# Optimization experiments

Hardware: AMD Instinct MI355X
Metric: run time of the kernel (lower is better)

Reference implementation:

```python
import jax, jax.numpy as jnp
import numpy as np

B = 64            # decode batch (one new token per sequence)
H = 32            # query heads
HKV = 2           # kv heads (multi_query_group_num)
D = 128           # head_size (kv_channels)
HID = 4096        # hidden size
ROT = D // 2      # ChatGLM applies rotary to first half of head dims
BLOCK = 16        # paged-cache block size
NBLK = 16384      # total blocks
MAX_S = 4096
ROPE_BASE = 10000.0


def setup_inputs() -> dict:
    key = jax.random.key(0)
    ks = jax.random.split(key, 8)
    hidden_states = jax.random.normal(ks[0], (B, HID), jnp.float32)
    wqkv = jax.random.normal(ks[1], (H * D + 2 * HKV * D, HID), jnp.float32) * 0.02
    wdense = jax.random.normal(ks[2], (HID, H * D), jnp.float32) * 0.02
    k_cache = jax.random.normal(ks[3], (NBLK, BLOCK, HKV, D), jnp.float32)
    v_cache = jax.random.normal(ks[4], (NBLK, BLOCK, HKV, D), jnp.float32)
    # disjoint block tables: sequence b owns blocks [b*256, (b+1)*256)
    block_tables = jnp.arange(B * (MAX_S // BLOCK), dtype=jnp.int32).reshape(B, MAX_S // BLOCK)
    input_lengths = jax.random.randint(ks[5], (B,), 1024, MAX_S + 1, dtype=jnp.int32)
    # slot of the current token = position input_lengths-1 within its block table
    pos = input_lengths - 1
    slots = block_tables[jnp.arange(B), pos // BLOCK] * BLOCK + pos % BLOCK
    return {"hidden_states": hidden_states, "wqkv": wqkv, "wdense": wdense,
            "k_cache": k_cache, "v_cache": v_cache, "block_tables": block_tables,
            "slots": slots, "input_lengths": input_lengths, "max_s": MAX_S}


def _apply_rope(x, positions):
    # x: [B, h, D]; GPT-J interleaved rope on first ROT dims (ChatGLM style)
    inv_freq = 1.0 / (ROPE_BASE ** (jnp.arange(0, ROT, 2, dtype=jnp.float32) / ROT))  # [ROT/2]
    ang = positions.astype(jnp.float32)[:, None] * inv_freq[None, :]                  # [B, ROT/2]
    c = jnp.cos(ang)[:, None, :]  # [B,1,ROT/2]
    s = jnp.sin(ang)[:, None, :]
    xr = x[..., :ROT].reshape(*x.shape[:-1], ROT // 2, 2)
    x0, x1 = xr[..., 0], xr[..., 1]
    rot = jnp.stack([x0 * c - x1 * s, x1 * c + x0 * s], axis=-1).reshape(*x.shape[:-1], ROT)
    return jnp.concatenate([rot, x[..., ROT:]], axis=-1)


def reference(hidden_states, wqkv, wdense, k_cache, v_cache, block_tables, slots, input_lengths, max_s):
    G = H // HKV
    scale = D ** -0.5
    positions = input_lengths - 1

    qkv = hidden_states @ wqkv.T                                   # [B, 4608]
    q, k, v = jnp.split(qkv, [H * D, H * D + HKV * D], axis=1)
    q = q.reshape(B, H, D)
    k = k.reshape(B, HKV, D)
    v = v.reshape(B, HKV, D)

    q = _apply_rope(q, positions)
    k = _apply_rope(k, positions)

    # reshape_and_cache: scatter current token's K/V into the paged cache
    kc = k_cache.reshape(NBLK * BLOCK, HKV, D).at[slots].set(k)
    vc = v_cache.reshape(NBLK * BLOCK, HKV, D).at[slots].set(v)

    # paged attention: gather per-sequence KV via block tables
    s_idx = jnp.arange(max_s)
    flat = block_tables[:, s_idx // BLOCK] * BLOCK + s_idx % BLOCK  # [B, S]
    K = kc[flat]                                                    # [B, S, HKV, D]
    V = vc[flat]

    q4 = q.reshape(B, HKV, G, D).astype(jnp.float32)
    scores = jnp.einsum('bkgd,bskd->bkgs', q4, K.astype(jnp.float32)) * scale  # [B,HKV,G,S]
    mask = s_idx[None, :] < input_lengths[:, None]                  # [B, S]
    scores = jnp.where(mask[:, None, None, :], scores, -jnp.inf)
    probs = jax.nn.softmax(scores, axis=-1)
    out = jnp.einsum('bkgs,bskd->bkgd', probs, V.astype(jnp.float32))  # [B,HKV,G,D]
    out = out.reshape(B, H * D).astype(hidden_states.dtype)
    return out @ wdense.T
```

## Files before the change

kernel.cpp:

```cpp
#include <hip/hip_runtime.h>
#include <math.h>

#define KDIM 4096
#define SPLITS 8
#define WAYS 32
#define MAXPB 256
#define NQKV 4608
#define NDENSE 4096
#define KSPLIT 8
#define KRANGE 512

typedef __attribute__((ext_vector_type(8))) short bh8;
typedef __attribute__((ext_vector_type(4))) float f32x4;

__device__ __forceinline__ short f2bf(float x) {
    union { float f; unsigned u; } v; v.f = x;
    unsigned r = v.u + 0x7FFFu + ((v.u >> 16) & 1u);
    return (short)(r >> 16);
}
__device__ __forceinline__ float bf2f(short h) {
    union { unsigned u; float f; } v;
    v.u = ((unsigned)(unsigned short)h) << 16;
    return v.f;
}

__device__ __forceinline__ void rope_rotate(float& x0, float& x1, int j, int pos) {
    double inv = pow(10000.0, -(double)j / 32.0);
    double ang = (double)pos * inv;
    float c = (float)cos(ang), s = (float)sin(ang);
    float r0 = x0 * c - x1 * s;
    float r1 = x1 * c + x0 * s;
    x0 = r0; x1 = r1;
}

__global__ __launch_bounds__(256) void prep_hilo(
    const float* __restrict__ x, unsigned short* __restrict__ hi,
    unsigned short* __restrict__ lo)
{
    const int i = (blockIdx.x * 256 + threadIdx.x) * 4;
    float4 v = *(const float4*)&x[i];
    unsigned short h4[4], l4[4];
    float vf[4] = {v.x, v.y, v.z, v.w};
    #pragma unroll
    for (int j = 0; j < 4; ++j) {
        short hh = f2bf(vf[j]);
        h4[j] = (unsigned short)hh;
        l4[j] = (unsigned short)f2bf(vf[j] - bf2f(hh));
    }
    *(ushort4*)&hi[i] = make_ushort4(h4[0], h4[1], h4[2], h4[3]);
    *(ushort4*)&lo[i] = make_ushort4(l4[0], l4[1], l4[2], l4[3]);
}

__global__ __launch_bounds__(256) void gemm_mfma(
    const unsigned short* __restrict__ A_hi, const unsigned short* __restrict__ A_lo,
    const float* __restrict__ W, float* __restrict__ part, int N)
{
    const int tid = threadIdx.x;
    const int wv = tid >> 6;
    const int l = tid & 63;
    const int lr = l & 15;
    const int h = l >> 4;
    const int n0 = blockIdx.x * 64 + wv * 16;
    const int k0 = blockIdx.y * KRANGE;

    const float* wrow = &W[(size_t)(n0 + lr) * KDIM + h * 8];
    const unsigned short* pah[4];
    const unsigned short* pal[4];
    #pragma unroll
    for (int mt = 0; mt < 4; ++mt) {
        pah[mt] = &A_hi[(mt * 16 + lr) * KDIM + h * 8];
        pal[mt] = &A_lo[(mt * 16 + lr) * KDIM + h * 8];
    }

    f32x4 acc[4];
    #pragma unroll
    for (int mt = 0; mt < 4; ++mt) acc[mt] = (f32x4){0.f, 0.f, 0.f, 0.f};

    float4 wc0, wc1, wn0, wn1;
    bh8 ahc[4], alc[4], ahn[4], aln[4];

    wc0 = *(const float4*)&wrow[k0];
    wc1 = *(const float4*)&wrow[k0 + 4];
    #pragma unroll
    for (int mt = 0; mt < 4; ++mt) {
        ahc[mt] = *(const bh8*)&pah[mt][k0];
        alc[mt] = *(const bh8*)&pal[mt][k0];
    }

    for (int kt = 0; kt < KRANGE / 32; ++kt) {
        if (kt + 1 < KRANGE / 32) {
            const int kn = k0 + (kt + 1) * 32;
            wn0 = *(const float4*)&wrow[kn];
            wn1 = *(const float4*)&wrow[kn + 4];
            #pragma unroll
            for (int mt = 0; mt < 4; ++mt) {
                ahn[mt] = *(const bh8*)&pah[mt][kn];
                aln[mt] = *(const bh8*)&pal[mt][kn];
            }
        }
        bh8 whi, wlo;
        float wf[8] = {wc0.x, wc0.y, wc0.z, wc0.w, wc1.x, wc1.y, wc1.z, wc1.w};
        #pragma unroll
        for (int e = 0; e < 8; ++e) {
            short hh = f2bf(wf[e]);
            whi[e] = hh;
            wlo[e] = f2bf(wf[e] - bf2f(hh));
        }
        #pragma unroll
        for (int mt = 0; mt < 4; ++mt) {
            acc[mt] = __builtin_amdgcn_mfma_f32_16x16x32_bf16(ahc[mt], whi, acc[mt], 0, 0, 0);
            acc[mt] = __builtin_amdgcn_mfma_f32_16x16x32_bf16(alc[mt], whi, acc[mt], 0, 0, 0);
            acc[mt] = __builtin_amdgcn_mfma_f32_16x16x32_bf16(ahc[mt], wlo, acc[mt], 0, 0, 0);
        }
        wc0 = wn0; wc1 = wn1;
        #pragma unroll
        for (int mt = 0; mt < 4; ++mt) { ahc[mt] = ahn[mt]; alc[mt] = aln[mt]; }
    }

    const int ks = blockIdx.y;
    #pragma unroll
    for (int mt = 0; mt < 4; ++mt) {
        const int m = mt * 16 + h * 4;
        #pragma unroll
        for (int j = 0; j < 4; ++j)
            part[((size_t)ks * 64 + m + j) * N + n0 + lr] = acc[mt][j];
    }
}

__global__ __launch_bounds__(256) void reduce_qkv(
    const float* __restrict__ part, const int* __restrict__ lens,
    float* __restrict__ q_rope, float* __restrict__ knew, float* __restrict__ vnew)
{
    const int b = blockIdx.y;
    const int c0 = (blockIdx.x * 256 + threadIdx.x) * 2;
    float x0 = 0.f, x1 = 0.f;
    #pragma unroll
    for (int ks = 0; ks < KSPLIT; ++ks) {
        float2 v = *(const float2*)&part[((size_t)ks * 64 + b) * NQKV + c0];
        x0 += v.x; x1 += v.y;
    }
    const int pos = lens[b] - 1;
    if (c0 < 4096) {
        const int d = c0 & 127;
        if (d < 64) rope_rotate(x0, x1, d >> 1, pos);
        q_rope[(size_t)b * 4096 + c0] = x0;
        q_rope[(size_t)b * 4096 + c0 + 1] = x1;
    } else if (c0 < 4352) {
        const int kidx = c0 - 4096, kh = kidx >> 7, d = kidx & 127;
        if (d < 64) rope_rotate(x0, x1, d >> 1, pos);
        knew[(b * 2 + kh) * 128 + d] = x0;
        knew[(b * 2 + kh) * 128 + d + 1] = x1;
    } else {
        const int vidx = c0 - 4352, kh = vidx >> 7, d = vidx & 127;
        vnew[(b * 2 + kh) * 128 + d] = x0;
        vnew[(b * 2 + kh) * 128 + d + 1] = x1;
    }
}

__global__ __launch_bounds__(256) void attn_mfma(
    const float* __restrict__ qr, const float* __restrict__ knew,
    const float* __restrict__ vnew, const float* __restrict__ kcache,
    const float* __restrict__ vcache, const int* __restrict__ bt,
    const int* __restrict__ lens, float* __restrict__ pO, float* __restrict__ pML)
{
    const int split = blockIdx.x;
    const int kh = blockIdx.y;
    const int b = blockIdx.z;
    const int tid = threadIdx.x;
    const int wv = tid >> 6;
    const int l = tid & 63;
    const int g = l & 15;
    const int h = l >> 4;
    const int way = split * 4 + wv;

    __shared__ unsigned int sP[4][256];
    __shared__ float sO[3][16][132];
    __shared__ float sML[3][2][16];

    const int len = lens[b];
    const int nchunks = (len + 31) >> 5;
    const size_t nbase = ((size_t)(b * 2 + kh)) * 128;

    const float scale = 0.08838834764831845f;
    bh8 qf[4];
    {
        const float* qrow = &qr[((size_t)(b * 32 + kh * 16 + g)) * 128 + h * 8];
        #pragma unroll
        for (int dc = 0; dc < 4; ++dc) {
            float4 a = *(const float4*)&qrow[dc * 32];
            float4 c = *(const float4*)&qrow[dc * 32 + 4];
            qf[dc][0] = f2bf(a.x * scale); qf[dc][1] = f2bf(a.y * scale);
            qf[dc][2] = f2bf(a.z * scale); qf[dc][3] = f2bf(a.w * scale);
            qf[dc][4] = f2bf(c.x * scale); qf[dc][5] = f2bf(c.y * scale);
            qf[dc][6] = f2bf(c.z * scale); qf[dc][7] = f2bf(c.w * scale);
        }
    }

    float m = -INFINITY, lacc = 0.f;
    f32x4 oacc[8];
    #pragma unroll
    for (int dt = 0; dt < 8; ++dt) oacc[dt] = (f32x4){0.f, 0.f, 0.f, 0.f};

    for (int c = way; c < nchunks; c += WAYS) {
        const int s0 = c * 32;
        const int blk0 = bt[b * MAXPB + 2 * c];
        const int blk1 = bt[b * MAXPB + 2 * c + 1];

        const float* rowK0 = (s0 + g == len - 1) ? &knew[nbase]
            : &kcache[(((size_t)blk0 * 16 + g) * 2 + kh) * 128];
        const float* rowK1 = (s0 + 16 + g == len - 1) ? &knew[nbase]
            : &kcache[(((size_t)blk1 * 16 + g) * 2 + kh) * 128];
        float4 k0[8], k1[8];
        #pragma unroll
        for (int dc = 0; dc < 4; ++dc) {
            k0[2*dc]   = *(const float4*)&rowK0[dc * 32 + h * 8];
            k0[2*dc+1] = *(const float4*)&rowK0[dc * 32 + h * 8 + 4];
            k1[2*dc]   = *(const float4*)&rowK1[dc * 32 + h * 8];
            k1[2*dc+1] = *(const float4*)&rowK1[dc * 32 + h * 8 + 4];
        }

        float vv[8][8];
        #pragma unroll
        for (int e = 0; e < 8; ++e) {
            const int p = h * 8 + e;
            const int s = s0 + p;
            const float* rowV = (s == len - 1) ? &vnew[nbase]
                : &vcache[(((size_t)(p < 16 ? blk0 : blk1) * 16 + (p & 15)) * 2 + kh) * 128];
            #pragma unroll
            for (int dt = 0; dt < 8; ++dt)
                vv[e][dt] = rowV[dt * 16 + g];
        }

        f32x4 sa0 = (f32x4){0.f,0.f,0.f,0.f};
        f32x4 sa1 = (f32x4){0.f,0.f,0.f,0.f};
        #pragma unroll
        for (int dc = 0; dc < 4; ++dc) {
            bh8 a0, a1;
            a0[0]=f2bf(k0[2*dc].x);   a0[1]=f2bf(k0[2*dc].y);
            a0[2]=f2bf(k0[2*dc].z);   a0[3]=f2bf(k0[2*dc].w);
            a0[4]=f2bf(k0[2*dc+1].x); a0[5]=f2bf(k0[2*dc+1].y);
            a0[6]=f2bf(k0[2*dc+1].z); a0[7]=f2bf(k0[2*dc+1].w);
            a1[0]=f2bf(k1[2*dc].x);   a1[1]=f2bf(k1[2*dc].y);
            a1[2]=f2bf(k1[2*dc].z);   a1[3]=f2bf(k1[2*dc].w);
            a1[4]=f2bf(k1[2*dc+1].x); a1[5]=f2bf(k1[2*dc+1].y);
            a1[6]=f2bf(k1[2*dc+1].z); a1[7]=f2bf(k1[2*dc+1].w);
            sa0 = __builtin_amdgcn_mfma_f32_16x16x32_bf16(a0, qf[dc], sa0, 0, 0, 0);
            sa1 = __builtin_amdgcn_mfma_f32_16x16x32_bf16(a1, qf[dc], sa1, 0, 0, 0);
        }

        float sc[8];
        #pragma unroll
        for (int j = 0; j < 4; ++j) {
            sc[j]     = (s0 + 4*h + j      < len) ? sa0[j] : -INFINITY;
            sc[4 + j] = (s0 + 16 + 4*h + j < len) ? sa1[j] : -INFINITY;
        }
        float tmax = sc[0];
        #pragma unroll
        for (int j = 1; j < 8; ++j) tmax = fmaxf(tmax, sc[j]);
        tmax = fmaxf(tmax, __shfl_xor(tmax, 16));
        tmax = fmaxf(tmax, __shfl_xor(tmax, 32));
        const float m_new = fmaxf(m, tmax);
        const float corr = expf(m - m_new);
        float pe[8], ls = 0.f;
        #pragma unroll
        for (int j = 0; j < 8; ++j) { pe[j] = expf(sc[j] - m_new); ls += pe[j]; }
        ls += __shfl_xor(ls, 16);
        ls += __shfl_xor(ls, 32);
        lacc = lacc * corr + ls;
        m = m_new;
        #pragma unroll
        for (int dt = 0; dt < 8; ++dt) {
            oacc[dt][0] *= corr; oacc[dt][1] *= corr;
            oacc[dt][2] *= corr; oacc[dt][3] *= corr;
        }

        unsigned int* myP = sP[wv];
        #pragma unroll
        for (int ph = 0; ph < 2; ++ph)
            #pragma unroll
            for (int t2 = 0; t2 < 2; ++t2) {
                unsigned lo = (unsigned short)f2bf(pe[ph*4 + 2*t2]);
                unsigned hi = (unsigned short)f2bf(pe[ph*4 + 2*t2 + 1]);
                myP[g * 16 + ph * 8 + 2 * h + t2] = lo | (hi << 16);
            }
        asm volatile("s_waitcnt lgkmcnt(0)" ::: "memory");
        bh8 pf = *(const bh8*)&myP[g * 16 + 4 * h];

        #pragma unroll
        for (int dt = 0; dt < 8; ++dt) {
            bh8 av;
            #pragma unroll
            for (int e = 0; e < 8; ++e) av[e] = f2bf(vv[e][dt]);
            oacc[dt] = __builtin_amdgcn_mfma_f32_16x16x32_bf16(av, pf, oacc[dt], 0, 0, 0);
        }
    }

    if (wv > 0) {
        #pragma unroll
        for (int dt = 0; dt < 8; ++dt)
            #pragma unroll
            for (int j = 0; j < 4; ++j)
                sO[wv-1][g][dt*16 + 4*h + j] = oacc[dt][j];
        if (l < 16) {
            sML[wv-1][0][g] = m;
            sML[wv-1][1][g] = lacc;
        }
    }
    __syncthreads();
    if (wv == 0) {
        float M = m;
        #pragma unroll
        for (int i = 0; i < 3; ++i) M = fmaxf(M, sML[i][0][g]);
        const float w0 = expf(m - M);
        float L = lacc * w0;
        float wi[3];
        #pragma unroll
        for (int i = 0; i < 3; ++i) {
            wi[i] = expf(sML[i][0][g] - M);
            L += sML[i][1][g] * wi[i];
        }
        size_t base = ((((size_t)(b * 2 + kh)) * SPLITS + split) * 16 + g) * 128;
        #pragma unroll
        for (int dt = 0; dt < 8; ++dt)
            #pragma unroll
            for (int j = 0; j < 4; ++j) {
                float o = oacc[dt][j] * w0;
                #pragma unroll
                for (int i = 0; i < 3; ++i)
                    o += sO[i][g][dt*16 + 4*h + j] * wi[i];
                pO[base + dt*16 + 4*h + j] = o;
            }
        if (l < 16) {
            size_t mb = ((((size_t)(b * 2 + kh)) * SPLITS + split) * 16 + g) * 2;
            pML[mb] = M;
            pML[mb + 1] = L;
        }
    }
}

__global__ __launch_bounds__(256) void attn_combine(
    const float* __restrict__ pO, const float* __restrict__ pML,
    unsigned short* __restrict__ a_hi, unsigned short* __restrict__ a_lo)
{
    const int bk = blockIdx.x;
    const int tid = threadIdx.x;
    const int g = tid >> 4;
    const int dh = tid & 15;

    float ms[SPLITS], ls[SPLITS];
    float M = -INFINITY;
    #pragma unroll
    for (int s = 0; s < SPLITS; ++s) {
        size_t mb = (((size_t)bk * SPLITS + s) * 16 + g) * 2;
        ms[s] = pML[mb]; ls[s] = pML[mb + 1];
        M = fmaxf(M, ms[s]);
    }
    float L = 0.f;
    #pragma unroll
    for (int s = 0; s < SPLITS; ++s) L += ls[s] * expf(ms[s] - M);

    float acc[8] = {0, 0, 0, 0, 0, 0, 0, 0};
    #pragma unroll
    for (int s = 0; s < SPLITS; ++s) {
        float wgt = expf(ms[s] - M);
        const float* src = &pO[(((size_t)bk * SPLITS + s) * 16 + g) * 128 + dh * 8];
        #pragma unroll
        for (int r = 0; r < 8; ++r) acc[r] += wgt * src[r];
    }
    const float invL = 1.f / L;
    const int b = bk >> 1, kh = bk & 1;
    const size_t idx = (size_t)b * 4096 + (kh * 16 + g) * 128 + dh * 8;
    unsigned short hbuf[8], lbuf[8];
    #pragma unroll
    for (int r = 0; r < 8; ++r) {
        float o = acc[r] * invL;
        short hh = f2bf(o);
        hbuf[r] = (unsigned short)hh;
        lbuf[r] = (unsigned short)f2bf(o - bf2f(hh));
    }
    *(int4*)&a_hi[idx] = *(int4*)hbuf;
    *(int4*)&a_lo[idx] = *(int4*)lbuf;
}

__global__ __launch_bounds__(256) void reduce_dense(
    const float* __restrict__ part, float* __restrict__ out)
{
    const int b = blockIdx.y;
    const int col = (blockIdx.x * 256 + threadIdx.x) * 4;
    float4 s = make_float4(0.f, 0.f, 0.f, 0.f);
    #pragma unroll
    for (int ks = 0; ks < KSPLIT; ++ks) {
        float4 v = *(const float4*)&part[((size_t)ks * 64 + b) * NDENSE + col];
        s.x += v.x; s.y += v.y; s.z += v.z; s.w += v.w;
    }
    *(float4*)&out[(size_t)b * 4096 + col] = s;
}

extern "C" void kernel_launch(void* const* d_in, const int* in_sizes, int n_in,
                              void* d_out, int out_size, void* d_ws, size_t ws_size,
                              hipStream_t stream) {
    const float* hidden = (const float*)d_in[0];
    const float* wqkv   = (const float*)d_in[1];
    const float* wdense = (const float*)d_in[2];
    const float* kcache = (const float*)d_in[3];
    const float* vcache = (const float*)d_in[4];
    const int*   bt     = (const int*)d_in[5];
    const int*   lens   = (const int*)d_in[7];
    float* out = (float*)d_out;

    float* ws     = (float*)d_ws;
    float* q_rope = ws;
    float* k_new  = ws + 262144;
    float* v_new  = ws + 278528;
    unsigned short* hiloA = (unsigned short*)(ws + 294912);
    unsigned short* A_hi = hiloA;
    unsigned short* A_lo = hiloA + 262144;
    float* regX   = ws + 557056;
    float* pO     = regX;
    float* pML    = ws + 2916352;

    prep_hilo<<<dim3(256), dim3(256), 0, stream>>>(hidden, A_hi, A_lo);
    gemm_mfma<<<dim3(NQKV / 64, KSPLIT), dim3(256), 0, stream>>>(
        A_hi, A_lo, wqkv, regX, NQKV);
    reduce_qkv<<<dim3(9, 64), dim3(256), 0, stream>>>(
        regX, lens, q_rope, k_new, v_new);
    attn_mfma<<<dim3(SPLITS, 2, 64), dim3(256), 0, stream>>>(
        q_rope, k_new, v_new, kcache, vcache, bt, lens, pO, pML);
    attn_combine<<<dim3(128), dim3(256), 0, stream>>>(pO, pML, A_hi, A_lo);
    gemm_mfma<<<dim3(NDENSE / 64, KSPLIT), dim3(256), 0, stream>>>(
        A_hi, A_lo, wdense, regX, NDENSE);
    reduce_dense<<<dim3(4, 64), dim3(256), 0, stream>>>(regX, out);
}
```

Measured before the change: 211.5 us.

## Pre-pack activations in MFMA fragment order and double split-K for GEMMs

After: 169.7 us (median of 2 runs). -19.7%, faster.

```diff
diff --git a/kernel.cpp b/kernel.cpp
--- a/kernel.cpp
+++ b/kernel.cpp
@@ -7,8 +7,8 @@
 #define MAXPB 256
 #define NQKV 4608
 #define NDENSE 4096
-#define KSPLIT 8
-#define KRANGE 512
+#define KSPLIT 16
+#define KRANGE 256
 
 typedef __attribute__((ext_vector_type(8))) short bh8;
 typedef __attribute__((ext_vector_type(4))) float f32x4;
@@ -33,22 +33,30 @@
     x0 = r0; x1 = r1;
 }
 
-__global__ __launch_bounds__(256) void prep_hilo(
+__global__ __launch_bounds__(256) void prep_hilo_pk(
     const float* __restrict__ x, unsigned short* __restrict__ hi,
     unsigned short* __restrict__ lo)
 {
-    const int i = (blockIdx.x * 256 + threadIdx.x) * 4;
-    float4 v = *(const float4*)&x[i];
-    unsigned short h4[4], l4[4];
-    float vf[4] = {v.x, v.y, v.z, v.w};
-    #pragma unroll
-    for (int j = 0; j < 4; ++j) {
-        short hh = f2bf(vf[j]);
-        h4[j] = (unsigned short)hh;
-        l4[j] = (unsigned short)f2bf(vf[j] - bf2f(hh));
-    }
-    *(ushort4*)&hi[i] = make_ushort4(h4[0], h4[1], h4[2], h4[3]);
-    *(ushort4*)&lo[i] = make_ushort4(l4[0], l4[1], l4[2], l4[3]);
+    const int id = blockIdx.x * 256 + threadIdx.x;
+    const int lane = id & 63;
+    const int mtkt = id >> 6;
+    const int mt = mtkt & 3;
+    const int kt = mtkt >> 2;
+    const int m = mt * 16 + (lane & 15);
+    const int kk = kt * 32 + (lane >> 4) * 8;
+    const float* src = &x[(size_t)m * KDIM + kk];
+    float4 a = *(const float4*)src;
+    float4 b = *(const float4*)(src + 4);
+    float vf[8] = {a.x, a.y, a.z, a.w, b.x, b.y, b.z, b.w};
+    unsigned short hbuf[8], lbuf[8];
+    #pragma unroll
+    for (int e = 0; e < 8; ++e) {
+        short hh = f2bf(vf[e]);
+        hbuf[e] = (unsigned short)hh;
+        lbuf[e] = (unsigned short)f2bf(vf[e] - bf2f(hh));
+    }
+    *(int4*)&hi[(size_t)id * 8] = *(int4*)hbuf;
+    *(int4*)&lo[(size_t)id * 8] = *(int4*)lbuf;
 }
 
 __global__ __launch_bounds__(256) void gemm_mfma(
@@ -61,45 +69,45 @@
     const int lr = l & 15;
     const int h = l >> 4;
     const int n0 = blockIdx.x * 64 + wv * 16;
-    const int k0 = blockIdx.y * KRANGE;
+    const int ks = blockIdx.y;
+    const int k0 = ks * KRANGE;
 
     const float* wrow = &W[(size_t)(n0 + lr) * KDIM + h * 8];
-    const unsigned short* pah[4];
-    const unsigned short* pal[4];
+    const size_t abase = (size_t)ks * 8 * 4 * 512 + (size_t)l * 8;
+
+    f32x4 acc[4];
+    #pragma unroll
+    for (int mt = 0; mt < 4; ++mt) acc[mt] = (f32x4){0.f, 0.f, 0.f, 0.f};
+
+    float4 w00, w01, w10, w11;
+    bh8 ahc[4], alc[4], ahn[4], aln[4];
+
+    w00 = *(const float4*)&wrow[k0];
+    w01 = *(const float4*)&wrow[k0 + 4];
+    w10 = *(const float4*)&wrow[k0 + 32];
+    w11 = *(const float4*)&wrow[k0 + 36];
     #pragma unroll
     for (int mt = 0; mt < 4; ++mt) {
-        pah[mt] = &A_hi[(mt * 16 + lr) * KDIM + h * 8];
-        pal[mt] = &A_lo[(mt * 16 + lr) * KDIM + h * 8];
-    }
-
-    f32x4 acc[4];
-    #pragma unroll
-    for (int mt = 0; mt < 4; ++mt) acc[mt] = (f32x4){0.f, 0.f, 0.f, 0.f};
-
-    float4 wc0, wc1, wn0, wn1;
-    bh8 ahc[4], alc[4], ahn[4], aln[4];
-
-    wc0 = *(const float4*)&wrow[k0];
-    wc1 = *(const float4*)&wrow[k0 + 4];
-    #pragma unroll
-    for (int mt = 0; mt < 4; ++mt) {
-        ahc[mt] = *(const bh8*)&pah[mt][k0];
-        alc[mt] = *(const bh8*)&pal[mt][k0];
-    }
-
-    for (int kt = 0; kt < KRANGE / 32; ++kt) {
-        if (kt + 1 < KRANGE / 32) {
-            const int kn = k0 + (kt + 1) * 32;
-            wn0 = *(const float4*)&wrow[kn];
-            wn1 = *(const float4*)&wrow[kn + 4];
+        ahc[mt] = *(const bh8*)&A_hi[abase + (size_t)mt * 512];
+        alc[mt] = *(const bh8*)&A_lo[abase + (size_t)mt * 512];
+    }
+
+    auto body = [&](float4& pwa, float4& pwb, int kt) {
+        float4 cw0 = pwa, cw1 = pwb;
+        if (kt + 2 < 8) {
+            pwa = *(const float4*)&wrow[k0 + (kt + 2) * 32];
+            pwb = *(const float4*)&wrow[k0 + (kt + 2) * 32 + 4];
+        }
+        if (kt + 1 < 8) {
+            const size_t an = abase + (size_t)(kt + 1) * 2048;
             #pragma unroll
             for (int mt = 0; mt < 4; ++mt) {
-                ahn[mt] = *(const bh8*)&pah[mt][kn];
-                aln[mt] = *(const bh8*)&pal[mt][kn];
+                ahn[mt] = *(const bh8*)&A_hi[an + (size_t)mt * 512];
+                aln[mt] = *(const bh8*)&A_lo[an + (size_t)mt * 512];
             }
         }
         bh8 whi, wlo;
-        float wf[8] = {wc0.x, wc0.y, wc0.z, wc0.w, wc1.x, wc1.y, wc1.z, wc1.w};
+        float wf[8] = {cw0.x, cw0.y, cw0.z, cw0.w, cw1.x, cw1.y, cw1.z, cw1.w};
         #pragma unroll
         for (int e = 0; e < 8; ++e) {
             short hh = f2bf(wf[e]);
@@ -112,12 +120,17 @@
             acc[mt] = __builtin_amdgcn_mfma_f32_16x16x32_bf16(alc[mt], whi, acc[mt], 0, 0, 0);
             acc[mt] = __builtin_amdgcn_mfma_f32_16x16x32_bf16(ahc[mt], wlo, acc[mt], 0, 0, 0);
         }
-        wc0 = wn0; wc1 = wn1;
-        #pragma unroll
-        for (int mt = 0; mt < 4; ++mt) { ahc[mt] = ahn[mt]; alc[mt] = aln[mt]; }
-    }
-
-    const int ks = blockIdx.y;
+        if (kt + 1 < 8) {
+            #pragma unroll
+            for (int mt = 0; mt < 4; ++mt) { ahc[mt] = ahn[mt]; alc[mt] = aln[mt]; }
+        }
+    };
+
+    for (int kt2 = 0; kt2 < 4; ++kt2) {
+        body(w00, w01, kt2 * 2);
+        body(w10, w11, kt2 * 2 + 1);
+    }
+
     #pragma unroll
     for (int mt = 0; mt < 4; ++mt) {
         const int m = mt * 16 + h * 4;
@@ -369,7 +382,10 @@
     }
     const float invL = 1.f / L;
     const int b = bk >> 1, kh = bk & 1;
-    const size_t idx = (size_t)b * 4096 + (kh * 16 + g) * 128 + dh * 8;
+    const int k0 = (kh * 16 + g) * 128 + dh * 8;
+    const int kt = k0 >> 5;
+    const int h2 = dh & 3;
+    const size_t didx = (((size_t)(kt * 4 + (b >> 4))) * 64 + h2 * 16 + (b & 15)) * 8;
     unsigned short hbuf[8], lbuf[8];
     #pragma unroll
     for (int r = 0; r < 8; ++r) {
@@ -378,8 +394,8 @@
         hbuf[r] = (unsigned short)hh;
         lbuf[r] = (unsigned short)f2bf(o - bf2f(hh));
     }
-    *(int4*)&a_hi[idx] = *(int4*)hbuf;
-    *(int4*)&a_lo[idx] = *(int4*)lbuf;
+    *(int4*)&a_hi[didx] = *(int4*)hbuf;
+    *(int4*)&a_lo[didx] = *(int4*)lbuf;
 }
 
 __global__ __launch_bounds__(256) void reduce_dense(
@@ -412,14 +428,13 @@
     float* q_rope = ws;
     float* k_new  = ws + 262144;
     float* v_new  = ws + 278528;
-    unsigned short* hiloA = (unsigned short*)(ws + 294912);
-    unsigned short* A_hi = hiloA;
-    unsigned short* A_lo = hiloA + 262144;
+    unsigned short* A_hi = (unsigned short*)(ws + 294912);
+    unsigned short* A_lo = A_hi + 262144;
     float* regX   = ws + 557056;
     float* pO     = regX;
-    float* pML    = ws + 2916352;
-
-    prep_hilo<<<dim3(256), dim3(256), 0, stream>>>(hidden, A_hi, A_lo);
+    float* pML    = ws + 5275648;
+
+    prep_hilo_pk<<<dim3(128), dim3(256), 0, stream>>>(hidden, A_hi, A_lo);
     gemm_mfma<<<dim3(NQKV / 64, KSPLIT), dim3(256), 0, stream>>>(
         A_hi, A_lo, wqkv, regX, NQKV);
     reduce_qkv<<<dim3(9, 64), dim3(256), 0, stream>>>(
```
